# Kernel optimization log

Hardware: AMD Instinct MI355X
Metric: run time of the kernel (lower is better)

Reference implementation:

```python
import jax, jax.numpy as jnp
import numpy as np

CANVAS = 28      # canvas_size
P = 2            # num_paths
S = 3            # num_segments
PPP = S * 3 + 1  # points_per_path = 10
T = 32           # samples per bezier segment
SS = 2           # 2x2 = 4 supersamples per pixel (num_samples=4)
MARGIN = 2.0
TAU = 0.5        # anti-alias softness of coverage (differentiable rasterizer)
LATENT = 64
HIDDEN = 512


def _leaky(x):
    return jnp.where(x >= 0, x, 0.2 * x)


def _encoder(x, e_w1, e_b1, e_w2, e_b2, w_mu, b_mu, w_lv, b_lv):
    h = x.reshape(x.shape[0], -1)
    h = _leaky(h @ e_w1 + e_b1)
    h = _leaky(h @ e_w2 + e_b2)
    return h @ w_mu + b_mu, h @ w_lv + b_lv


def _decoder(z, d_w1, d_b1, d_w2, d_b2, p_w, p_b, wd_w, wd_b, a_w, a_b):
    B = z.shape[0]
    h = jax.nn.selu(z @ d_w1 + d_b1)
    h = jax.nn.selu(h @ d_w2 + d_b2)
    pts = jnp.tanh(h @ p_w + p_b).reshape(B, P, PPP, 2)
    pts = pts * (CANVAS / 2 - MARGIN) + CANVAS / 2
    # stack overlapping cubic segments: [B,P,S,4,2]
    cp = jnp.stack([pts[:, :, 3 * s:3 * s + 4, :] for s in range(S)], axis=2)
    widths = jax.nn.sigmoid(h @ wd_w + wd_b) * 2.0 + 1.0  # [B,P]
    alphas = jax.nn.sigmoid(h @ a_w + a_b)                # [B,P]
    return cp, widths, alphas


def _render(cp, widths, alphas):
    """Differentiable supersampled stroke rasterizer, white bg, 1-x flip."""
    B = cp.shape[0]
    t = (jnp.arange(T, dtype=cp.dtype) + 0.5) / T
    basis = jnp.stack([(1 - t) ** 3, 3 * t * (1 - t) ** 2,
                       3 * t ** 2 * (1 - t), t ** 3], axis=-1)  # [T,4]
    curve = jnp.einsum('tk,bpskc->bpstc', basis, cp).reshape(B, P, S * T, 2)
    # supersampled pixel sample positions (pixel units)
    coords = (jnp.arange(CANVAS * SS, dtype=cp.dtype) + 0.5) / SS
    ys, xs = jnp.meshgrid(coords, coords, indexing='ij')
    samp = jnp.stack([xs, ys], -1).reshape(-1, 2)  # [N,2], N = (28*2)^2
    # [B,P,N,M] squared distances -> min over curve samples
    d2 = jnp.sum((samp[None, None, :, None, :] - curve[:, :, None, :, :]) ** 2, -1)
    d = jnp.sqrt(jnp.min(d2, axis=-1) + 1e-12)  # [B,P,N]
    cov = jax.nn.sigmoid((widths[..., None] * 0.5 - d) / TAU)
    a = alphas[..., None] * cov                 # per-path ink opacity
    val = jnp.prod(1.0 - a, axis=1)             # composite black ink over bg=1.0
    img = val.reshape(B, CANVAS, SS, CANVAS, SS).mean(axis=(2, 4))
    return 1.0 - img[:, None]                   # [B,1,H,W]


def setup_inputs() -> dict:
    key = jax.random.key(0)
    ks = jax.random.split(key, 24)
    n = lambda k, s, sc=0.05: (jax.random.normal(k, s, dtype=jnp.float32) * sc)
    B = 128
    return {
        'x': jax.random.uniform(ks[0], (B, 1, 28, 28), dtype=jnp.float32),
        'eps': jax.random.normal(ks[1], (B, LATENT), dtype=jnp.float32),
        'e_w1': n(ks[2], (784, 256)), 'e_b1': jnp.zeros(256),
        'e_w2': n(ks[3], (256, 256)), 'e_b2': jnp.zeros(256),
        'w_mu': n(ks[4], (256, LATENT)), 'b_mu': jnp.zeros(LATENT),
        'w_lv': n(ks[5], (256, LATENT)), 'b_lv': jnp.zeros(LATENT),
        'd_w1': n(ks[6], (LATENT, HIDDEN)), 'd_b1': jnp.zeros(HIDDEN),
        'd_w2': n(ks[7], (HIDDEN, HIDDEN)), 'd_b2': jnp.zeros(HIDDEN),
        'p_w': n(ks[8], (HIDDEN, P * PPP * 2)), 'p_b': jnp.zeros(P * PPP * 2),
        'wd_w': n(ks[9], (HIDDEN, P)), 'wd_b': jnp.zeros(P),
        'a_w': n(ks[10], (HIDDEN, P)), 'a_b': jnp.zeros(P),
    }


def reference(x, eps, e_w1, e_b1, e_w2, e_b2, w_mu, b_mu, w_lv, b_lv,
              d_w1, d_b1, d_w2, d_b2, p_w, p_b, wd_w, wd_b, a_w, a_b):
    mu, logvar = _encoder(x, e_w1, e_b1, e_w2, e_b2, w_mu, b_mu, w_lv, b_lv)
    z = mu + eps * jnp.exp(0.5 * logvar)
    cp, widths, alphas = _decoder(z, d_w1, d_b1, d_w2, d_b2,
                                  p_w, p_b, wd_w, wd_b, a_w, a_b)
    rendered = _render(cp, widths, alphas)
    return rendered, mu, logvar, cp, widths, alphas
```

## Files before the change

kernel.cpp:

```cpp
#include <hip/hip_runtime.h>
#include <hip/hip_bf16.h>
#include <hip/hip_fp16.h>
#include <math.h>

#define REND_OFF 0
#define MU_OFF   100352
#define LV_OFF   108544
#define CP_OFF   116736
#define W_OFF    122880
#define A_OFF    123136

#define Q_W1 0
#define Q_W2 25600
#define Q_ML 33792
#define Q_D1 37888
#define Q_D2 41984
#define Q_H  74752
#define Q_TOT 78848

typedef _Float16 half2_t __attribute__((ext_vector_type(2)));

__device__ __forceinline__ float leakyf(float x) {
    return x >= 0.f ? x : 0.2f * x;
}
__device__ __forceinline__ float seluf(float x) {
    const float sc = 1.0507009873554805f;
    const float al = 1.6732632423543772f;
    return x > 0.f ? sc * x : sc * al * expm1f(x);
}
__device__ __forceinline__ float sigmoidf(float x) {
    return 1.f / (1.f + expf(-x));
}
__device__ __forceinline__ unsigned pkh(float a, float b) {
    __half ha = __float2half(a), hb = __float2half(b);
    return (unsigned)__half_as_ushort(ha) | ((unsigned)__half_as_ushort(hb) << 16);
}
__device__ __forceinline__ half2_t as_h2(unsigned u) {
    union { unsigned u; half2_t h; } c; c.u = u; return c.h;
}
__device__ __forceinline__ float dot2(unsigned a, unsigned w, float acc) {
#if __has_builtin(__builtin_amdgcn_fdot2)
    return __builtin_amdgcn_fdot2(as_h2(a), as_h2(w), acc, false);
#else
    half2_t ah = as_h2(a), wh = as_h2(w);
    acc = fmaf((float)ah[0], (float)wh[0], acc);
    return fmaf((float)ah[1], (float)wh[1], acc);
#endif
}

__global__ __launch_bounds__(256) void conv_w(
    const float* __restrict__ e_w1, const float* __restrict__ e_w2,
    const float* __restrict__ w_mu, const float* __restrict__ w_lv,
    const float* __restrict__ d_w1, const float* __restrict__ d_w2,
    const float* __restrict__ p_w,  const float* __restrict__ wd_w,
    const float* __restrict__ a_w,  uint4* __restrict__ wsq)
{
    int t = blockIdx.x * 256 + threadIdx.x;
    if (t >= Q_TOT) return;
    float lo[4], hi[4];
    if (t < Q_W2) {
        int q = t, k2 = q >> 6, j4 = q & 63;
        int k0 = 2 * k2, c0 = 4 * j4;
        #pragma unroll
        for (int c = 0; c < 4; ++c) {
            lo[c] = (k0     < 784) ? e_w1[k0 * 256 + c0 + c] : 0.f;
            hi[c] = (k0 + 1 < 784) ? e_w1[(k0 + 1) * 256 + c0 + c] : 0.f;
        }
    } else if (t < Q_ML) {
        int q = t - Q_W2, k2 = q >> 6, j4 = q & 63;
        int k0 = 2 * k2, c0 = 4 * j4;
        #pragma unroll
        for (int c = 0; c < 4; ++c) {
            lo[c] = e_w2[k0 * 256 + c0 + c];
            hi[c] = e_w2[(k0 + 1) * 256 + c0 + c];
        }
    } else if (t < Q_D1) {
        int q = t - Q_ML, k2 = q >> 5, j4 = q & 31;
        int k0 = 2 * k2, c0 = 4 * j4;
        #pragma unroll
        for (int c = 0; c < 4; ++c) {
            int cc = c0 + c;
            lo[c] = (cc < 64) ? w_mu[k0 * 64 + cc] : w_lv[k0 * 64 + cc - 64];
            hi[c] = (cc < 64) ? w_mu[(k0 + 1) * 64 + cc]
                              : w_lv[(k0 + 1) * 64 + cc - 64];
        }
    } else if (t < Q_D2) {
        int q = t - Q_D1, k2 = q >> 7, j4 = q & 127;
        int k0 = 2 * k2, c0 = 4 * j4;
        #pragma unroll
        for (int c = 0; c < 4; ++c) {
            lo[c] = d_w1[k0 * 512 + c0 + c];
            hi[c] = d_w1[(k0 + 1) * 512 + c0 + c];
        }
    } else if (t < Q_H) {
        int q = t - Q_D2, k2 = q >> 7, j4 = q & 127;
        int k0 = 2 * k2, c0 = 4 * j4;
        #pragma unroll
        for (int c = 0; c < 4; ++c) {
            lo[c] = d_w2[k0 * 512 + c0 + c];
            hi[c] = d_w2[(k0 + 1) * 512 + c0 + c];
        }
    } else {
        int q = t - Q_H, k2 = q >> 4, j4 = q & 15;
        int k0 = 2 * k2, c0 = 4 * j4;
        #pragma unroll
        for (int c = 0; c < 4; ++c) {
            int cc = c0 + c;
            lo[c] = (cc < 40) ? p_w[k0 * 40 + cc]
                  : (cc < 42) ? wd_w[k0 * 2 + cc - 40]
                  : (cc < 44) ? a_w[k0 * 2 + cc - 42] : 0.f;
            hi[c] = (cc < 40) ? p_w[(k0 + 1) * 40 + cc]
                  : (cc < 42) ? wd_w[(k0 + 1) * 2 + cc - 40]
                  : (cc < 44) ? a_w[(k0 + 1) * 2 + cc - 42] : 0.f;
        }
    }
    uint4 u;
    u.x = pkh(lo[0], hi[0]);
    u.y = pkh(lo[1], hi[1]);
    u.z = pkh(lo[2], hi[2]);
    u.w = pkh(lo[3], hi[3]);
    wsq[t] = u;
}

template<int N, int JG, int S, int Ks>
__device__ __forceinline__ void hgemm(const uint4* __restrict__ wq,
                                      const unsigned* __restrict__ xu,
                                      float* __restrict__ red, int tid)
{
    constexpr int NTp = N + 4;
    const int jg = tid % JG, ks = tid / JG;
    const uint4* wp = wq + (ks * Ks) * (N / 4) + jg;
    const unsigned* xp = xu + ks * Ks;
    float a0 = 0.f, a1 = 0.f, a2 = 0.f, a3 = 0.f;
    #pragma unroll 8
    for (int kk = 0; kk < Ks; ++kk) {
        uint4 w = wp[kk * (N / 4)];
        unsigned av = xp[kk];
        a0 = dot2(av, w.x, a0);
        a1 = dot2(av, w.y, a1);
        a2 = dot2(av, w.z, a2);
        a3 = dot2(av, w.w, a3);
    }
    *(float4*)&red[ks * NTp + 4 * jg] = make_float4(a0, a1, a2, a3);
}

template<int N, int S, int ACT>
__device__ __forceinline__ void reduce_pack(const float* __restrict__ red,
                                            const float* __restrict__ bias,
                                            unsigned* __restrict__ Cu, int tid)
{
    constexpr int NTp = N + 4;
    if (tid < N / 2) {
        int j0 = 2 * tid;
        float s0 = bias[j0], s1 = bias[j0 + 1];
        #pragma unroll
        for (int si = 0; si < S; ++si) {
            s0 += red[si * NTp + j0];
            s1 += red[si * NTp + j0 + 1];
        }
        if (ACT == 1) { s0 = leakyf(s0); s1 = leakyf(s1); }
        else          { s0 = seluf(s0);  s1 = seluf(s1);  }
        Cu[tid] = pkh(s0, s1);
    }
}

__global__ __launch_bounds__(1024) void vae_mlp(
    const float* __restrict__ x,    const float* __restrict__ eps,
    const float* __restrict__ e_b1, const float* __restrict__ e_b2,
    const float* __restrict__ b_mu, const float* __restrict__ b_lv,
    const float* __restrict__ d_b1, const float* __restrict__ d_b2,
    const float* __restrict__ p_b,  const float* __restrict__ wd_b,
    const float* __restrict__ a_b,
    const uint4* __restrict__ wsq,  float* __restrict__ out)
{
    const int b   = blockIdx.x;
    const int tid = threadIdx.x;

    __shared__ __align__(16) unsigned xs[400];
    __shared__ __align__(16) unsigned h1u[128];
    __shared__ __align__(16) unsigned h2u[128];
    __shared__ __align__(16) unsigned zu[32];
    __shared__ __align__(16) unsigned d1u[256];
    __shared__ __align__(16) unsigned d2u[256];
    __shared__ float mulv[128];
    __shared__ float pts[40];
    __shared__ __align__(16) float red[4352];

    if (tid < 400) {
        int k0 = 2 * tid;
        float x0 = (k0     < 784) ? x[b * 784 + k0] : 0.f;
        float x1 = (k0 + 1 < 784) ? x[b * 784 + k0 + 1] : 0.f;
        xs[tid] = pkh(x0, x1);
    }
    __syncthreads();

    hgemm<256, 64, 16, 25>(wsq + Q_W1, xs, red, tid);
    __syncthreads();
    reduce_pack<256, 16, 1>(red, e_b1, h1u, tid);
    __syncthreads();

    hgemm<256, 64, 16, 8>(wsq + Q_W2, h1u, red, tid);
    __syncthreads();
    reduce_pack<256, 16, 1>(red, e_b2, h2u, tid);
    __syncthreads();

    hgemm<128, 32, 32, 4>(wsq + Q_ML, h2u, red, tid);
    __syncthreads();
    if (tid < 64) {
        int u0 = 2 * tid;
        float s0 = (u0 < 64) ? b_mu[u0] : b_lv[u0 - 64];
        float s1 = (u0 < 64) ? b_mu[u0 + 1] : b_lv[u0 + 1 - 64];
        #pragma unroll
        for (int si = 0; si < 32; ++si) {
            s0 += red[si * 132 + u0];
            s1 += red[si * 132 + u0 + 1];
        }
        mulv[u0] = s0; mulv[u0 + 1] = s1;
        int base = (u0 < 64) ? MU_OFF : LV_OFF;
        out[base + b * 64 + (u0 & 63)]     = s0;
        out[base + b * 64 + (u0 & 63) + 1] = s1;
    }
    __syncthreads();
    if (tid < 32) {
        int j0 = 2 * tid;
        float z0 = fmaf(eps[b * 64 + j0],     expf(0.5f * mulv[64 + j0]),     mulv[j0]);
        float z1 = fmaf(eps[b * 64 + j0 + 1], expf(0.5f * mulv[64 + j0 + 1]), mulv[j0 + 1]);
        zu[tid] = pkh(z0, z1);
    }
    __syncthreads();

    hgemm<512, 128, 8, 4>(wsq + Q_D1, zu, red, tid);
    __syncthreads();
    reduce_pack<512, 8, 2>(red, d_b1, d1u, tid);
    __syncthreads();

    hgemm<512, 128, 8, 32>(wsq + Q_D2, d1u, red, tid);
    __syncthreads();
    reduce_pack<512, 8, 2>(red, d_b2, d2u, tid);
    __syncthreads();

    hgemm<64, 16, 64, 4>(wsq + Q_H, d2u, red, tid);
    __syncthreads();
    if (tid < 44) {
        float s = 0.f;
        #pragma unroll
        for (int si = 0; si < 64; ++si) s += red[si * 68 + tid];
        if (tid < 40) {
            pts[tid] = tanhf(s + p_b[tid]) * 12.f + 14.f;
        } else if (tid < 42) {
            out[W_OFF + b * 2 + (tid - 40)] =
                sigmoidf(s + wd_b[tid - 40]) * 2.f + 1.f;
        } else {
            out[A_OFF + b * 2 + (tid - 42)] = sigmoidf(s + a_b[tid - 42]);
        }
    }
    __syncthreads();

    if (tid < 48) {
        int p = tid / 24, rem = tid % 24;
        int s = rem / 8, kc = rem % 8;
        int k = kc >> 1, c = kc & 1;
        out[CP_OFF + b * 48 + tid] = pts[p * 20 + (3 * s + k) * 2 + c];
    }
}

__global__ __launch_bounds__(256) void vae_render(float* __restrict__ out)
{
    const int b   = blockIdx.x;
    const int q   = blockIdx.y;
    const int tid = threadIdx.x;

    __shared__ float2 cur[192];
    __shared__ float  wa[4];

    if (tid < 192) {
        int p = tid / 96;
        int m = tid % 96;
        int s = m / 32;
        int t = m % 32;
        float u  = (t + 0.5f) * (1.f / 32.f);
        float v  = 1.f - u;
        float b0 = v * v * v;
        float b1 = 3.f * u * v * v;
        float b2 = 3.f * u * u * v;
        float b3 = u * u * u;
        const float* cp = out + CP_OFF + b * 48 + p * 24 + s * 8;
        float cx = b0 * cp[0] + b1 * cp[2] + b2 * cp[4] + b3 * cp[6];
        float cy = b0 * cp[1] + b1 * cp[3] + b2 * cp[5] + b3 * cp[7];
        cur[tid] = make_float2(cx, cy);
    } else if (tid < 196) {
        int i = tid - 192;
        wa[i] = (i < 2) ? 0.5f * out[W_OFF + b * 2 + i]
                        : out[A_OFF + b * 2 + (i - 2)];
    }
    __syncthreads();

    if (tid < 196) {
        int Y = tid / 28, X = tid - Y * 28;
        float px0 = X + 0.25f;
        float py0 = (7 * q + Y) + 0.25f;

        float mA[4] = {1e30f, 1e30f, 1e30f, 1e30f};
        float mB[4] = {1e30f, 1e30f, 1e30f, 1e30f};
        #pragma unroll 4
        for (int m = 0; m < 96; ++m) {
            float2 c = cur[m];
            float dx0 = px0 - c.x, dy0 = py0 - c.y;
            float dx1 = dx0 + 0.5f, dy1 = dy0 + 0.5f;
            float xx0 = dx0 * dx0, xx1 = dx1 * dx1;
            float yy0 = dy0 * dy0, yy1 = dy1 * dy1;
            mA[0] = fminf(mA[0], xx0 + yy0);
            mA[1] = fminf(mA[1], xx1 + yy0);
            mA[2] = fminf(mA[2], xx0 + yy1);
            mA[3] = fminf(mA[3], xx1 + yy1);
        }
        #pragma unroll 4
        for (int m = 96; m < 192; ++m) {
            float2 c = cur[m];
            float dx0 = px0 - c.x, dy0 = py0 - c.y;
            float dx1 = dx0 + 0.5f, dy1 = dy0 + 0.5f;
            float xx0 = dx0 * dx0, xx1 = dx1 * dx1;
            float yy0 = dy0 * dy0, yy1 = dy1 * dy1;
            mB[0] = fminf(mB[0], xx0 + yy0);
            mB[1] = fminf(mB[1], xx1 + yy0);
            mB[2] = fminf(mB[2], xx0 + yy1);
            mB[3] = fminf(mB[3], xx1 + yy1);
        }

        const float w0 = wa[0], w1 = wa[1], a0 = wa[2], a1 = wa[3];
        float v = 0.f;
        #pragma unroll
        for (int s = 0; s < 4; ++s) {
            float d0 = sqrtf(mA[s] + 1e-12f);
            float d1 = sqrtf(mB[s] + 1e-12f);
            float c0 = a0 / (1.f + expf(-2.f * (w0 - d0)));
            float c1 = a1 / (1.f + expf(-2.f * (w1 - d1)));
            v += (1.f - c0) * (1.f - c1);
        }
        out[REND_OFF + b * 784 + (7 * q + Y) * 28 + X] = 1.f - 0.25f * v;
    }
}

extern "C" void kernel_launch(void* const* d_in, const int* in_sizes, int n_in,
                              void* d_out, int out_size, void* d_ws, size_t ws_size,
                              hipStream_t stream) {
    const float* x    = (const float*)d_in[0];
    const float* eps  = (const float*)d_in[1];
    const float* e_w1 = (const float*)d_in[2];
    const float* e_b1 = (const float*)d_in[3];
    const float* e_w2 = (const float*)d_in[4];
    const float* e_b2 = (const float*)d_in[5];
    const float* w_mu = (const float*)d_in[6];
    const float* b_mu = (const float*)d_in[7];
    const float* w_lv = (const float*)d_in[8];
    const float* b_lv = (const float*)d_in[9];
    const float* d_w1 = (const float*)d_in[10];
    const float* d_b1 = (const float*)d_in[11];
    const float* d_w2 = (const float*)d_in[12];
    const float* d_b2 = (const float*)d_in[13];
    const float* p_w  = (const float*)d_in[14];
    const float* p_b  = (const float*)d_in[15];
    const float* wd_w = (const float*)d_in[16];
    const float* wd_b = (const float*)d_in[17];
    const float* a_w  = (const float*)d_in[18];
    const float* a_b  = (const float*)d_in[19];
    float* out = (float*)d_out;
    uint4* wsq = (uint4*)d_ws;

    hipLaunchKernelGGL(conv_w, dim3((Q_TOT + 255) / 256), dim3(256), 0, stream,
                       e_w1, e_w2, w_mu, w_lv, d_w1, d_w2, p_w, wd_w, a_w, wsq);
    hipLaunchKernelGGL(vae_mlp, dim3(128), dim3(1024), 0, stream,
                       x, eps, e_b1, e_b2, b_mu, b_lv, d_b1, d_b2,
                       p_b, wd_b, a_b, wsq, out);
    hipLaunchKernelGGL(vae_render, dim3(128, 4), dim3(256), 0, stream, out);
}
```

Measured before the change: 123.7 us.

## Quantize MLP weights to per-column int8 instead of fp16 packed pairs

Replaces the fp16 weight conversion with a per-column symmetric int8 quantization kernel that stores a scale per output column, then runs the MLP GEMMs with unsigned-offset int8 weights against fp32 activations and corrects the offset using the activation sum. The aim is to halve the weight bytes each of the 128 blocks streams from cache/memory. In exchange, the inner loop does more ALU work: byte extraction, int-to-float converts and four scalar FMAs in place of each fdot2. The conversion kernel also gains a per-column max reduction, and int8 weights bring extra quantization error.

```diff
diff --git a/kernel.cpp b/kernel.cpp
--- a/kernel.cpp
+++ b/kernel.cpp
@@ -1,6 +1,4 @@
 #include <hip/hip_runtime.h>
-#include <hip/hip_bf16.h>
-#include <hip/hip_fp16.h>
 #include <math.h>
 
 #define REND_OFF 0
@@ -10,15 +8,20 @@
 #define W_OFF    122880
 #define A_OFF    123136
 
-#define Q_W1 0
-#define Q_W2 25600
-#define Q_ML 33792
-#define Q_D1 37888
-#define Q_D2 41984
-#define Q_H  74752
-#define Q_TOT 78848
-
-typedef _Float16 half2_t __attribute__((ext_vector_type(2)));
+#define U_W1 0
+#define U_W2 53248
+#define U_ML 69632
+#define U_D1 77824
+#define U_D2 86016
+#define U_H  151552
+#define SCOFF 159744
+#define B_W1 0
+#define B_W2 256
+#define B_ML 512
+#define B_D1 640
+#define B_D2 1152
+#define B_H  1664
+#define NCOLS 1728
 
 __device__ __forceinline__ float leakyf(float x) {
     return x >= 0.f ? x : 0.2f * x;
@@ -31,136 +34,109 @@
 __device__ __forceinline__ float sigmoidf(float x) {
     return 1.f / (1.f + expf(-x));
 }
-__device__ __forceinline__ unsigned pkh(float a, float b) {
-    __half ha = __float2half(a), hb = __float2half(b);
-    return (unsigned)__half_as_ushort(ha) | ((unsigned)__half_as_ushort(hb) << 16);
-}
-__device__ __forceinline__ half2_t as_h2(unsigned u) {
-    union { unsigned u; half2_t h; } c; c.u = u; return c.h;
-}
-__device__ __forceinline__ float dot2(unsigned a, unsigned w, float acc) {
-#if __has_builtin(__builtin_amdgcn_fdot2)
-    return __builtin_amdgcn_fdot2(as_h2(a), as_h2(w), acc, false);
-#else
-    half2_t ah = as_h2(a), wh = as_h2(w);
-    acc = fmaf((float)ah[0], (float)wh[0], acc);
-    return fmaf((float)ah[1], (float)wh[1], acc);
-#endif
-}
-
-__global__ __launch_bounds__(256) void conv_w(
+__device__ __forceinline__ float ub0(unsigned w) { return (float)(w & 0xffu); }
+__device__ __forceinline__ float ub1(unsigned w) { return (float)((w >> 8) & 0xffu); }
+__device__ __forceinline__ float ub2(unsigned w) { return (float)((w >> 16) & 0xffu); }
+__device__ __forceinline__ float ub3(unsigned w) { return (float)(w >> 24); }
+
+__global__ __launch_bounds__(256) void conv_q(
     const float* __restrict__ e_w1, const float* __restrict__ e_w2,
     const float* __restrict__ w_mu, const float* __restrict__ w_lv,
     const float* __restrict__ d_w1, const float* __restrict__ d_w2,
     const float* __restrict__ p_w,  const float* __restrict__ wd_w,
-    const float* __restrict__ a_w,  uint4* __restrict__ wsq)
-{
-    int t = blockIdx.x * 256 + threadIdx.x;
-    if (t >= Q_TOT) return;
-    float lo[4], hi[4];
-    if (t < Q_W2) {
-        int q = t, k2 = q >> 6, j4 = q & 63;
-        int k0 = 2 * k2, c0 = 4 * j4;
-        #pragma unroll
-        for (int c = 0; c < 4; ++c) {
-            lo[c] = (k0     < 784) ? e_w1[k0 * 256 + c0 + c] : 0.f;
-            hi[c] = (k0 + 1 < 784) ? e_w1[(k0 + 1) * 256 + c0 + c] : 0.f;
-        }
-    } else if (t < Q_ML) {
-        int q = t - Q_W2, k2 = q >> 6, j4 = q & 63;
-        int k0 = 2 * k2, c0 = 4 * j4;
-        #pragma unroll
-        for (int c = 0; c < 4; ++c) {
-            lo[c] = e_w2[k0 * 256 + c0 + c];
-            hi[c] = e_w2[(k0 + 1) * 256 + c0 + c];
-        }
-    } else if (t < Q_D1) {
-        int q = t - Q_ML, k2 = q >> 5, j4 = q & 31;
-        int k0 = 2 * k2, c0 = 4 * j4;
-        #pragma unroll
-        for (int c = 0; c < 4; ++c) {
-            int cc = c0 + c;
-            lo[c] = (cc < 64) ? w_mu[k0 * 64 + cc] : w_lv[k0 * 64 + cc - 64];
-            hi[c] = (cc < 64) ? w_mu[(k0 + 1) * 64 + cc]
-                              : w_lv[(k0 + 1) * 64 + cc - 64];
-        }
-    } else if (t < Q_D2) {
-        int q = t - Q_D1, k2 = q >> 7, j4 = q & 127;
-        int k0 = 2 * k2, c0 = 4 * j4;
-        #pragma unroll
-        for (int c = 0; c < 4; ++c) {
-            lo[c] = d_w1[k0 * 512 + c0 + c];
-            hi[c] = d_w1[(k0 + 1) * 512 + c0 + c];
-        }
-    } else if (t < Q_H) {
-        int q = t - Q_D2, k2 = q >> 7, j4 = q & 127;
-        int k0 = 2 * k2, c0 = 4 * j4;
-        #pragma unroll
-        for (int c = 0; c < 4; ++c) {
-            lo[c] = d_w2[k0 * 512 + c0 + c];
-            hi[c] = d_w2[(k0 + 1) * 512 + c0 + c];
-        }
-    } else {
-        int q = t - Q_H, k2 = q >> 4, j4 = q & 15;
-        int k0 = 2 * k2, c0 = 4 * j4;
-        #pragma unroll
-        for (int c = 0; c < 4; ++c) {
-            int cc = c0 + c;
-            lo[c] = (cc < 40) ? p_w[k0 * 40 + cc]
-                  : (cc < 42) ? wd_w[k0 * 2 + cc - 40]
-                  : (cc < 44) ? a_w[k0 * 2 + cc - 42] : 0.f;
-            hi[c] = (cc < 40) ? p_w[(k0 + 1) * 40 + cc]
-                  : (cc < 42) ? wd_w[(k0 + 1) * 2 + cc - 40]
-                  : (cc < 44) ? a_w[(k0 + 1) * 2 + cc - 42] : 0.f;
-        }
-    }
-    uint4 u;
-    u.x = pkh(lo[0], hi[0]);
-    u.y = pkh(lo[1], hi[1]);
-    u.z = pkh(lo[2], hi[2]);
-    u.w = pkh(lo[3], hi[3]);
-    wsq[t] = u;
-}
-
-template<int N, int JG, int S, int Ks>
-__device__ __forceinline__ void hgemm(const uint4* __restrict__ wq,
-                                      const unsigned* __restrict__ xu,
-                                      float* __restrict__ red, int tid)
+    const float* __restrict__ a_w,  unsigned* __restrict__ wsu)
+{
+    const int col  = blockIdx.x * 4 + (threadIdx.x >> 6);
+    const int lane = threadIdx.x & 63;
+    if (col >= NCOLS) return;
+
+    int K, G, N, base, c;
+    const float* src = nullptr;
+    int stride = 0;
+    if (col < 256)       { c = col;        K = 784; G = 208; N = 256; base = U_W1; src = e_w1 + c; stride = 256; }
+    else if (col < 512)  { c = col - 256;  K = 256; G = 64;  N = 256; base = U_W2; src = e_w2 + c; stride = 256; }
+    else if (col < 640)  { c = col - 512;  K = 256; G = 64;  N = 128; base = U_ML;
+                           src = (c < 64) ? (w_mu + c) : (w_lv + c - 64); stride = 64; }
+    else if (col < 1152) { c = col - 640;  K = 64;  G = 16;  N = 512; base = U_D1; src = d_w1 + c; stride = 512; }
+    else if (col < 1664) { c = col - 1152; K = 512; G = 128; N = 512; base = U_D2; src = d_w2 + c; stride = 512; }
+    else                 { c = col - 1664; K = 512; G = 128; N = 64;  base = U_H;
+                           if (c < 40)      { src = p_w + c;        stride = 40; }
+                           else if (c < 42) { src = wd_w + (c - 40); stride = 2; }
+                           else if (c < 44) { src = a_w + (c - 42);  stride = 2; }
+                           else             { src = nullptr; } }
+
+    float m = 0.f;
+    if (src) {
+        for (int k = lane; k < K; k += 64)
+            m = fmaxf(m, fabsf(src[k * stride]));
+    }
+    #pragma unroll
+    for (int d = 1; d < 64; d <<= 1)
+        m = fmaxf(m, __shfl_xor(m, d));
+    const float inv = (m > 0.f) ? 127.f / m : 0.f;
+    const float scale = m / 127.f;
+
+    const int colN = col - ((col < 256) ? 0 : (col < 512) ? 256 : (col < 640) ? 512
+                     : (col < 1152) ? 640 : (col < 1664) ? 1152 : 1664);
+    for (int g = lane; g < G; g += 64) {
+        unsigned u = 0;
+        #pragma unroll
+        for (int e = 0; e < 4; ++e) {
+            int k = 4 * g + e;
+            float w = (src && k < K) ? src[k * stride] : 0.f;
+            float qf = rintf(w * inv);
+            qf = fminf(127.f, fmaxf(-127.f, qf));
+            unsigned b = (unsigned)((int)qf + 128);
+            u |= b << (8 * e);
+        }
+        wsu[base + g * N + colN] = u;
+    }
+    if (lane == 0)
+        ((float*)(wsu + SCOFF))[col] = scale;
+}
+
+template<int N, int JG, int S, int G>
+__device__ __forceinline__ void i8gemm(const uint4* __restrict__ wq,
+                                       const float* __restrict__ xf,
+                                       float* __restrict__ red, int tid)
 {
     constexpr int NTp = N + 4;
     const int jg = tid % JG, ks = tid / JG;
-    const uint4* wp = wq + (ks * Ks) * (N / 4) + jg;
-    const unsigned* xp = xu + ks * Ks;
-    float a0 = 0.f, a1 = 0.f, a2 = 0.f, a3 = 0.f;
+    const uint4* wp = wq + (ks * G) * (N / 4) + jg;
+    const float4* xp = (const float4*)xf + ks * G;
+    float a0 = 0.f, a1 = 0.f, a2 = 0.f, a3 = 0.f, sx = 0.f;
     #pragma unroll 8
-    for (int kk = 0; kk < Ks; ++kk) {
-        uint4 w = wp[kk * (N / 4)];
-        unsigned av = xp[kk];
-        a0 = dot2(av, w.x, a0);
-        a1 = dot2(av, w.y, a1);
-        a2 = dot2(av, w.z, a2);
-        a3 = dot2(av, w.w, a3);
-    }
-    *(float4*)&red[ks * NTp + 4 * jg] = make_float4(a0, a1, a2, a3);
+    for (int g = 0; g < G; ++g) {
+        uint4 w = wp[g * (N / 4)];
+        float4 xv = xp[g];
+        sx += (xv.x + xv.y) + (xv.z + xv.w);
+        a0 = fmaf(ub0(w.x), xv.x, a0); a0 = fmaf(ub1(w.x), xv.y, a0);
+        a0 = fmaf(ub2(w.x), xv.z, a0); a0 = fmaf(ub3(w.x), xv.w, a0);
+        a1 = fmaf(ub0(w.y), xv.x, a1); a1 = fmaf(ub1(w.y), xv.y, a1);
+        a1 = fmaf(ub2(w.y), xv.z, a1); a1 = fmaf(ub3(w.y), xv.w, a1);
+        a2 = fmaf(ub0(w.z), xv.x, a2); a2 = fmaf(ub1(w.z), xv.y, a2);
+        a2 = fmaf(ub2(w.z), xv.z, a2); a2 = fmaf(ub3(w.z), xv.w, a2);
+        a3 = fmaf(ub0(w.w), xv.x, a3); a3 = fmaf(ub1(w.w), xv.y, a3);
+        a3 = fmaf(ub2(w.w), xv.z, a3); a3 = fmaf(ub3(w.w), xv.w, a3);
+    }
+    const float bias = -128.f * sx;
+    *(float4*)&red[ks * NTp + 4 * jg] =
+        make_float4(a0 + bias, a1 + bias, a2 + bias, a3 + bias);
 }
 
 template<int N, int S, int ACT>
-__device__ __forceinline__ void reduce_pack(const float* __restrict__ red,
-                                            const float* __restrict__ bias,
-                                            unsigned* __restrict__ Cu, int tid)
+__device__ __forceinline__ void reduce_i8(const float* __restrict__ red,
+                                          const float* __restrict__ scl,
+                                          const float* __restrict__ bias,
+                                          float* __restrict__ Cf, int tid)
 {
     constexpr int NTp = N + 4;
-    if (tid < N / 2) {
-        int j0 = 2 * tid;
-        float s0 = bias[j0], s1 = bias[j0 + 1];
-        #pragma unroll
-        for (int si = 0; si < S; ++si) {
-            s0 += red[si * NTp + j0];
-            s1 += red[si * NTp + j0 + 1];
-        }
-        if (ACT == 1) { s0 = leakyf(s0); s1 = leakyf(s1); }
-        else          { s0 = seluf(s0);  s1 = seluf(s1);  }
-        Cu[tid] = pkh(s0, s1);
+    if (tid < N) {
+        float s = 0.f;
+        #pragma unroll
+        for (int si = 0; si < S; ++si) s += red[si * NTp + tid];
+        float v = fmaf(scl[tid], s, bias[tid]);
+        Cf[tid] = (ACT == 1) ? leakyf(v) : seluf(v);
     }
 }
 
@@ -171,80 +147,71 @@
     const float* __restrict__ d_b1, const float* __restrict__ d_b2,
     const float* __restrict__ p_b,  const float* __restrict__ wd_b,
     const float* __restrict__ a_b,
-    const uint4* __restrict__ wsq,  float* __restrict__ out)
+    const unsigned* __restrict__ wsu, float* __restrict__ out)
 {
     const int b   = blockIdx.x;
     const int tid = threadIdx.x;
 
-    __shared__ __align__(16) unsigned xs[400];
-    __shared__ __align__(16) unsigned h1u[128];
-    __shared__ __align__(16) unsigned h2u[128];
-    __shared__ __align__(16) unsigned zu[32];
-    __shared__ __align__(16) unsigned d1u[256];
-    __shared__ __align__(16) unsigned d2u[256];
+    __shared__ __align__(16) float xs[832];
+    __shared__ __align__(16) float h1f[256];
+    __shared__ __align__(16) float h2f[256];
+    __shared__ __align__(16) float zf[64];
+    __shared__ __align__(16) float d1f[512];
+    __shared__ __align__(16) float d2f[512];
     __shared__ float mulv[128];
     __shared__ float pts[40];
+    __shared__ float scl[NCOLS];
     __shared__ __align__(16) float red[4352];
 
-    if (tid < 400) {
-        int k0 = 2 * tid;
-        float x0 = (k0     < 784) ? x[b * 784 + k0] : 0.f;
-        float x1 = (k0 + 1 < 784) ? x[b * 784 + k0 + 1] : 0.f;
-        xs[tid] = pkh(x0, x1);
-    }
-    __syncthreads();
-
-    hgemm<256, 64, 16, 25>(wsq + Q_W1, xs, red, tid);
-    __syncthreads();
-    reduce_pack<256, 16, 1>(red, e_b1, h1u, tid);
-    __syncthreads();
-
-    hgemm<256, 64, 16, 8>(wsq + Q_W2, h1u, red, tid);
-    __syncthreads();
-    reduce_pack<256, 16, 1>(red, e_b2, h2u, tid);
-    __syncthreads();
-
-    hgemm<128, 32, 32, 4>(wsq + Q_ML, h2u, red, tid);
+    if (tid < 832) xs[tid] = (tid < 784) ? x[b * 784 + tid] : 0.f;
+    for (int i = tid; i < NCOLS; i += 1024)
+        scl[i] = ((const float*)(wsu + SCOFF))[i];
+    __syncthreads();
+
+    i8gemm<256, 64, 16, 13>((const uint4*)(wsu + U_W1), xs, red, tid);
+    __syncthreads();
+    reduce_i8<256, 16, 1>(red, scl + B_W1, e_b1, h1f, tid);
+    __syncthreads();
+
+    i8gemm<256, 64, 16, 4>((const uint4*)(wsu + U_W2), h1f, red, tid);
+    __syncthreads();
+    reduce_i8<256, 16, 1>(red, scl + B_W2, e_b2, h2f, tid);
+    __syncthreads();
+
+    i8gemm<128, 32, 32, 2>((const uint4*)(wsu + U_ML), h2f, red, tid);
+    __syncthreads();
+    if (tid < 128) {
+        float s = 0.f;
+        #pragma unroll
+        for (int si = 0; si < 32; ++si) s += red[si * 132 + tid];
+        float v = fmaf(scl[B_ML + tid], s,
+                       (tid < 64) ? b_mu[tid] : b_lv[tid - 64]);
+        mulv[tid] = v;
+        out[(tid < 64 ? MU_OFF : LV_OFF) + b * 64 + (tid & 63)] = v;
+    }
     __syncthreads();
     if (tid < 64) {
-        int u0 = 2 * tid;
-        float s0 = (u0 < 64) ? b_mu[u0] : b_lv[u0 - 64];
-        float s1 = (u0 < 64) ? b_mu[u0 + 1] : b_lv[u0 + 1 - 64];
-        #pragma unroll
-        for (int si = 0; si < 32; ++si) {
-            s0 += red[si * 132 + u0];
-            s1 += red[si * 132 + u0 + 1];
-        }
-        mulv[u0] = s0; mulv[u0 + 1] = s1;
-        int base = (u0 < 64) ? MU_OFF : LV_OFF;
-        out[base + b * 64 + (u0 & 63)]     = s0;
-        out[base + b * 64 + (u0 & 63) + 1] = s1;
-    }
-    __syncthreads();
-    if (tid < 32) {
-        int j0 = 2 * tid;
-        float z0 = fmaf(eps[b * 64 + j0],     expf(0.5f * mulv[64 + j0]),     mulv[j0]);
-        float z1 = fmaf(eps[b * 64 + j0 + 1], expf(0.5f * mulv[64 + j0 + 1]), mulv[j0 + 1]);
-        zu[tid] = pkh(z0, z1);
-    }
-    __syncthreads();
-
-    hgemm<512, 128, 8, 4>(wsq + Q_D1, zu, red, tid);
-    __syncthreads();
-    reduce_pack<512, 8, 2>(red, d_b1, d1u, tid);
-    __syncthreads();
-
-    hgemm<512, 128, 8, 32>(wsq + Q_D2, d1u, red, tid);
-    __syncthreads();
-    reduce_pack<512, 8, 2>(red, d_b2, d2u, tid);
-    __syncthreads();
-
-    hgemm<64, 16, 64, 4>(wsq + Q_H, d2u, red, tid);
+        zf[tid] = fmaf(eps[b * 64 + tid], expf(0.5f * mulv[64 + tid]), mulv[tid]);
+    }
+    __syncthreads();
+
+    i8gemm<512, 128, 8, 2>((const uint4*)(wsu + U_D1), zf, red, tid);
+    __syncthreads();
+    reduce_i8<512, 8, 2>(red, scl + B_D1, d_b1, d1f, tid);
+    __syncthreads();
+
+    i8gemm<512, 128, 8, 16>((const uint4*)(wsu + U_D2), d1f, red, tid);
+    __syncthreads();
+    reduce_i8<512, 8, 2>(red, scl + B_D2, d_b2, d2f, tid);
+    __syncthreads();
+
+    i8gemm<64, 16, 64, 2>((const uint4*)(wsu + U_H), d2f, red, tid);
     __syncthreads();
     if (tid < 44) {
         float s = 0.f;
         #pragma unroll
         for (int si = 0; si < 64; ++si) s += red[si * 68 + tid];
+        s *= scl[B_H + tid];
         if (tid < 40) {
             pts[tid] = tanhf(s + p_b[tid]) * 12.f + 14.f;
         } else if (tid < 42) {
@@ -365,12 +332,12 @@
     const float* a_w  = (const float*)d_in[18];
     const float* a_b  = (const float*)d_in[19];
     float* out = (float*)d_out;
-    uint4* wsq = (uint4*)d_ws;
-
-    hipLaunchKernelGGL(conv_w, dim3((Q_TOT + 255) / 256), dim3(256), 0, stream,
-                       e_w1, e_w2, w_mu, w_lv, d_w1, d_w2, p_w, wd_w, a_w, wsq);
+    unsigned* wsu = (unsigned*)d_ws;
+
+    hipLaunchKernelGGL(conv_q, dim3(432), dim3(256), 0, stream,
+                       e_w1, e_w2, w_mu, w_lv, d_w1, d_w2, p_w, wd_w, a_w, wsu);
     hipLaunchKernelGGL(vae_mlp, dim3(128), dim3(1024), 0, stream,
                        x, eps, e_b1, e_b2, b_mu, b_lv, d_b1, d_b2,
-                       p_b, wd_b, a_b, wsq, out);
+                       p_b, wd_b, a_b, wsu, out);
     hipLaunchKernelGGL(vae_render, dim3(128, 4), dim3(256), 0, stream, out);
 }
```

New measurement: 133.9 us. 8.2% more time.

## Replace shared-memory split-K reduction with wave shuffle reductions in MLP kernel

Applied to the files above, without the earlier changes.

Each hgemm now gives a wavefront a group of output columns and splits K across the lanes of that wave, then reduces the partial sums with __shfl_xor butterflies instead of writing them to shared memory and running a separate reduce pass. This removes one __syncthreads and one LDS round trip per layer, and the bias vectors are preloaded into shared memory once at the start. In exchange, the shuffle steps add cross-lane traffic, and the per-lane weight access pattern changes, which may hurt coalescing.

```diff
diff --git a/kernel.cpp b/kernel.cpp
--- a/kernel.cpp
+++ b/kernel.cpp
@@ -17,6 +17,17 @@
 #define Q_D2 41984
 #define Q_H  74752
 #define Q_TOT 78848
+
+#define SB_E1 0
+#define SB_E2 256
+#define SB_MU 512
+#define SB_LV 576
+#define SB_D1 640
+#define SB_D2 1152
+#define SB_P  1664
+#define SB_WD 1704
+#define SB_A  1706
+#define SB_TOT 1708
 
 typedef _Float16 half2_t __attribute__((ext_vector_type(2)));
 
@@ -122,15 +133,17 @@
     wsq[t] = u;
 }
 
-template<int N, int JG, int S, int Ks>
-__device__ __forceinline__ void hgemm(const uint4* __restrict__ wq,
-                                      const unsigned* __restrict__ xu,
-                                      float* __restrict__ red, int tid)
+template<int N, int JW, int Ks>
+__device__ __forceinline__ void hgemm_w(const uint4* __restrict__ wq,
+                                        const unsigned* __restrict__ xu,
+                                        float (&a)[4], int tid)
 {
-    constexpr int NTp = N + 4;
-    const int jg = tid % JG, ks = tid / JG;
-    const uint4* wp = wq + (ks * Ks) * (N / 4) + jg;
-    const unsigned* xp = xu + ks * Ks;
+    const int l  = tid & 63;
+    const int wv = tid >> 6;
+    const int jg = wv * JW + (l % JW);
+    const int g  = l / JW;
+    const uint4* wp = wq + (g * Ks) * (N / 4) + jg;
+    const unsigned* xp = xu + g * Ks;
     float a0 = 0.f, a1 = 0.f, a2 = 0.f, a3 = 0.f;
     #pragma unroll 8
     for (int kk = 0; kk < Ks; ++kk) {
@@ -141,27 +154,14 @@
         a2 = dot2(av, w.z, a2);
         a3 = dot2(av, w.w, a3);
     }
-    *(float4*)&red[ks * NTp + 4 * jg] = make_float4(a0, a1, a2, a3);
-}
-
-template<int N, int S, int ACT>
-__device__ __forceinline__ void reduce_pack(const float* __restrict__ red,
-                                            const float* __restrict__ bias,
-                                            unsigned* __restrict__ Cu, int tid)
-{
-    constexpr int NTp = N + 4;
-    if (tid < N / 2) {
-        int j0 = 2 * tid;
-        float s0 = bias[j0], s1 = bias[j0 + 1];
-        #pragma unroll
-        for (int si = 0; si < S; ++si) {
-            s0 += red[si * NTp + j0];
-            s1 += red[si * NTp + j0 + 1];
-        }
-        if (ACT == 1) { s0 = leakyf(s0); s1 = leakyf(s1); }
-        else          { s0 = seluf(s0);  s1 = seluf(s1);  }
-        Cu[tid] = pkh(s0, s1);
-    }
+    #pragma unroll
+    for (int m = JW; m < 64; m <<= 1) {
+        a0 += __shfl_xor(a0, m);
+        a1 += __shfl_xor(a1, m);
+        a2 += __shfl_xor(a2, m);
+        a3 += __shfl_xor(a3, m);
+    }
+    a[0] = a0; a[1] = a1; a[2] = a2; a[3] = a3;
 }
 
 __global__ __launch_bounds__(1024) void vae_mlp(
@@ -175,6 +175,8 @@
 {
     const int b   = blockIdx.x;
     const int tid = threadIdx.x;
+    const int l   = tid & 63;
+    const int wv  = tid >> 6;
 
     __shared__ __align__(16) unsigned xs[400];
     __shared__ __align__(16) unsigned h1u[128];
@@ -184,7 +186,7 @@
     __shared__ __align__(16) unsigned d2u[256];
     __shared__ float mulv[128];
     __shared__ float pts[40];
-    __shared__ __align__(16) float red[4352];
+    __shared__ float sb[SB_TOT];
 
     if (tid < 400) {
         int k0 = 2 * tid;
@@ -192,33 +194,53 @@
         float x1 = (k0 + 1 < 784) ? x[b * 784 + k0 + 1] : 0.f;
         xs[tid] = pkh(x0, x1);
     }
-    __syncthreads();
-
-    hgemm<256, 64, 16, 25>(wsq + Q_W1, xs, red, tid);
-    __syncthreads();
-    reduce_pack<256, 16, 1>(red, e_b1, h1u, tid);
-    __syncthreads();
-
-    hgemm<256, 64, 16, 8>(wsq + Q_W2, h1u, red, tid);
-    __syncthreads();
-    reduce_pack<256, 16, 1>(red, e_b2, h2u, tid);
-    __syncthreads();
-
-    hgemm<128, 32, 32, 4>(wsq + Q_ML, h2u, red, tid);
-    __syncthreads();
-    if (tid < 64) {
-        int u0 = 2 * tid;
-        float s0 = (u0 < 64) ? b_mu[u0] : b_lv[u0 - 64];
-        float s1 = (u0 < 64) ? b_mu[u0 + 1] : b_lv[u0 + 1 - 64];
-        #pragma unroll
-        for (int si = 0; si < 32; ++si) {
-            s0 += red[si * 132 + u0];
-            s1 += red[si * 132 + u0 + 1];
-        }
-        mulv[u0] = s0; mulv[u0 + 1] = s1;
-        int base = (u0 < 64) ? MU_OFF : LV_OFF;
-        out[base + b * 64 + (u0 & 63)]     = s0;
-        out[base + b * 64 + (u0 & 63) + 1] = s1;
+    for (int i = tid; i < SB_TOT; i += 1024) {
+        float v;
+        if (i < 256)       v = e_b1[i];
+        else if (i < 512)  v = e_b2[i - 256];
+        else if (i < 576)  v = b_mu[i - 512];
+        else if (i < 640)  v = b_lv[i - 576];
+        else if (i < 1152) v = d_b1[i - 640];
+        else if (i < 1664) v = d_b2[i - 1152];
+        else if (i < 1704) v = p_b[i - 1664];
+        else if (i < 1706) v = wd_b[i - 1704];
+        else               v = a_b[i - 1706];
+        sb[i] = v;
+    }
+    __syncthreads();
+
+    float a[4];
+
+    hgemm_w<256, 4, 25>(wsq + Q_W1, xs, a, tid);
+    if (l < 4) {
+        int jg = wv * 4 + l, c0 = 4 * jg;
+        h1u[2 * jg]     = pkh(leakyf(a[0] + sb[SB_E1 + c0]),
+                              leakyf(a[1] + sb[SB_E1 + c0 + 1]));
+        h1u[2 * jg + 1] = pkh(leakyf(a[2] + sb[SB_E1 + c0 + 2]),
+                              leakyf(a[3] + sb[SB_E1 + c0 + 3]));
+    }
+    __syncthreads();
+
+    hgemm_w<256, 4, 8>(wsq + Q_W2, h1u, a, tid);
+    if (l < 4) {
+        int jg = wv * 4 + l, c0 = 4 * jg;
+        h2u[2 * jg]     = pkh(leakyf(a[0] + sb[SB_E2 + c0]),
+                              leakyf(a[1] + sb[SB_E2 + c0 + 1]));
+        h2u[2 * jg + 1] = pkh(leakyf(a[2] + sb[SB_E2 + c0 + 2]),
+                              leakyf(a[3] + sb[SB_E2 + c0 + 3]));
+    }
+    __syncthreads();
+
+    hgemm_w<128, 2, 4>(wsq + Q_ML, h2u, a, tid);
+    if (l < 2) {
+        int jg = wv * 2 + l, c0 = 4 * jg;
+        #pragma unroll
+        for (int e = 0; e < 4; ++e) {
+            int cc = c0 + e;
+            float v = a[e] + ((cc < 64) ? sb[SB_MU + cc] : sb[SB_LV + cc - 64]);
+            mulv[cc] = v;
+            out[((cc < 64) ? MU_OFF : LV_OFF) + b * 64 + (cc & 63)] = v;
+        }
     }
     __syncthreads();
     if (tid < 32) {
@@ -229,29 +251,41 @@
     }
     __syncthreads();
 
-    hgemm<512, 128, 8, 4>(wsq + Q_D1, zu, red, tid);
-    __syncthreads();
-    reduce_pack<512, 8, 2>(red, d_b1, d1u, tid);
-    __syncthreads();
-
-    hgemm<512, 128, 8, 32>(wsq + Q_D2, d1u, red, tid);
-    __syncthreads();
-    reduce_pack<512, 8, 2>(red, d_b2, d2u, tid);
-    __syncthreads();
-
-    hgemm<64, 16, 64, 4>(wsq + Q_H, d2u, red, tid);
-    __syncthreads();
-    if (tid < 44) {
-        float s = 0.f;
-        #pragma unroll
-        for (int si = 0; si < 64; ++si) s += red[si * 68 + tid];
-        if (tid < 40) {
-            pts[tid] = tanhf(s + p_b[tid]) * 12.f + 14.f;
-        } else if (tid < 42) {
-            out[W_OFF + b * 2 + (tid - 40)] =
-                sigmoidf(s + wd_b[tid - 40]) * 2.f + 1.f;
-        } else {
-            out[A_OFF + b * 2 + (tid - 42)] = sigmoidf(s + a_b[tid - 42]);
+    hgemm_w<512, 8, 4>(wsq + Q_D1, zu, a, tid);
+    if (l < 8) {
+        int jg = wv * 8 + l, c0 = 4 * jg;
+        d1u[2 * jg]     = pkh(seluf(a[0] + sb[SB_D1 + c0]),
+                              seluf(a[1] + sb[SB_D1 + c0 + 1]));
+        d1u[2 * jg + 1] = pkh(seluf(a[2] + sb[SB_D1 + c0 + 2]),
+                              seluf(a[3] + sb[SB_D1 + c0 + 3]));
+    }
+    __syncthreads();
+
+    hgemm_w<512, 8, 32>(wsq + Q_D2, d1u, a, tid);
+    if (l < 8) {
+        int jg = wv * 8 + l, c0 = 4 * jg;
+        d2u[2 * jg]     = pkh(seluf(a[0] + sb[SB_D2 + c0]),
+                              seluf(a[1] + sb[SB_D2 + c0 + 1]));
+        d2u[2 * jg + 1] = pkh(seluf(a[2] + sb[SB_D2 + c0 + 2]),
+                              seluf(a[3] + sb[SB_D2 + c0 + 3]));
+    }
+    __syncthreads();
+
+    hgemm_w<64, 1, 4>(wsq + Q_H, d2u, a, tid);
+    if (l == 0) {
+        int c0 = 4 * wv;
+        #pragma unroll
+        for (int e = 0; e < 4; ++e) {
+            int cc = c0 + e;
+            if (cc < 40) {
+                pts[cc] = tanhf(a[e] + sb[SB_P + cc]) * 12.f + 14.f;
+            } else if (cc < 42) {
+                out[W_OFF + b * 2 + (cc - 40)] =
+                    sigmoidf(a[e] + sb[SB_WD + cc - 40]) * 2.f + 1.f;
+            } else if (cc < 44) {
+                out[A_OFF + b * 2 + (cc - 42)] =
+                    sigmoidf(a[e] + sb[SB_A + cc - 42]);
+            }
         }
     }
     __syncthreads();
```

After: 127.2 us. +2.8%, slower.

## Fuse stroke rendering into the MLP kernel to drop the render launch

Applied to the files above, without the earlier changes.

Moves the Bezier curve evaluation and supersampled rendering into the tail of the per-sample MLP kernel. Curve points and width/alpha values now come straight from shared memory instead of being re-read from global output. Each 1024-thread block renders all 784 pixels itself. This removes one kernel launch and the global round-trip, at the cost of fewer blocks doing the render work (128 instead of 512) and a bigger shared-memory footprint for the MLP kernel.

```diff
diff --git a/kernel.cpp b/kernel.cpp
--- a/kernel.cpp
+++ b/kernel.cpp
@@ -184,7 +184,9 @@
     __shared__ __align__(16) unsigned d2u[256];
     __shared__ float mulv[128];
     __shared__ float pts[40];
+    __shared__ float wa[4];
     __shared__ __align__(16) float red[4352];
+    __shared__ float2 cur[192];
 
     if (tid < 400) {
         int k0 = 2 * tid;
@@ -248,10 +250,13 @@
         if (tid < 40) {
             pts[tid] = tanhf(s + p_b[tid]) * 12.f + 14.f;
         } else if (tid < 42) {
-            out[W_OFF + b * 2 + (tid - 40)] =
-                sigmoidf(s + wd_b[tid - 40]) * 2.f + 1.f;
+            float wd = sigmoidf(s + wd_b[tid - 40]) * 2.f + 1.f;
+            out[W_OFF + b * 2 + (tid - 40)] = wd;
+            wa[tid - 40] = 0.5f * wd;
         } else {
-            out[A_OFF + b * 2 + (tid - 42)] = sigmoidf(s + a_b[tid - 42]);
+            float al = sigmoidf(s + a_b[tid - 42]);
+            out[A_OFF + b * 2 + (tid - 42)] = al;
+            wa[tid - 42 + 2] = al;
         }
     }
     __syncthreads();
@@ -262,43 +267,27 @@
         int k = kc >> 1, c = kc & 1;
         out[CP_OFF + b * 48 + tid] = pts[p * 20 + (3 * s + k) * 2 + c];
     }
-}
-
-__global__ __launch_bounds__(256) void vae_render(float* __restrict__ out)
-{
-    const int b   = blockIdx.x;
-    const int q   = blockIdx.y;
-    const int tid = threadIdx.x;
-
-    __shared__ float2 cur[192];
-    __shared__ float  wa[4];
-
-    if (tid < 192) {
-        int p = tid / 96;
-        int m = tid % 96;
-        int s = m / 32;
-        int t = m % 32;
+    if (tid >= 64 && tid < 256) {
+        int i = tid - 64;
+        int p = i / 96, m = i % 96;
+        int s = m / 32, t = m % 32;
         float u  = (t + 0.5f) * (1.f / 32.f);
         float v  = 1.f - u;
         float b0 = v * v * v;
         float b1 = 3.f * u * v * v;
         float b2 = 3.f * u * u * v;
         float b3 = u * u * u;
-        const float* cp = out + CP_OFF + b * 48 + p * 24 + s * 8;
-        float cx = b0 * cp[0] + b1 * cp[2] + b2 * cp[4] + b3 * cp[6];
-        float cy = b0 * cp[1] + b1 * cp[3] + b2 * cp[5] + b3 * cp[7];
-        cur[tid] = make_float2(cx, cy);
-    } else if (tid < 196) {
-        int i = tid - 192;
-        wa[i] = (i < 2) ? 0.5f * out[W_OFF + b * 2 + i]
-                        : out[A_OFF + b * 2 + (i - 2)];
-    }
-    __syncthreads();
-
-    if (tid < 196) {
+        const float* q = pts + p * 20 + 3 * s * 2;
+        float cx = b0 * q[0] + b1 * q[2] + b2 * q[4] + b3 * q[6];
+        float cy = b0 * q[1] + b1 * q[3] + b2 * q[5] + b3 * q[7];
+        cur[i] = make_float2(cx, cy);
+    }
+    __syncthreads();
+
+    if (tid < 784) {
         int Y = tid / 28, X = tid - Y * 28;
         float px0 = X + 0.25f;
-        float py0 = (7 * q + Y) + 0.25f;
+        float py0 = Y + 0.25f;
 
         float mA[4] = {1e30f, 1e30f, 1e30f, 1e30f};
         float mB[4] = {1e30f, 1e30f, 1e30f, 1e30f};
@@ -327,17 +316,17 @@
             mB[3] = fminf(mB[3], xx1 + yy1);
         }
 
-        const float w0 = wa[0], w1 = wa[1], a0 = wa[2], a1 = wa[3];
+        const float w0 = wa[0], w1 = wa[1], al0 = wa[2], al1 = wa[3];
         float v = 0.f;
         #pragma unroll
         for (int s = 0; s < 4; ++s) {
             float d0 = sqrtf(mA[s] + 1e-12f);
             float d1 = sqrtf(mB[s] + 1e-12f);
-            float c0 = a0 / (1.f + expf(-2.f * (w0 - d0)));
-            float c1 = a1 / (1.f + expf(-2.f * (w1 - d1)));
+            float c0 = al0 / (1.f + expf(-2.f * (w0 - d0)));
+            float c1 = al1 / (1.f + expf(-2.f * (w1 - d1)));
             v += (1.f - c0) * (1.f - c1);
         }
-        out[REND_OFF + b * 784 + (7 * q + Y) * 28 + X] = 1.f - 0.25f * v;
+        out[REND_OFF + b * 784 + Y * 28 + X] = 1.f - 0.25f * v;
     }
 }
 
@@ -372,5 +361,4 @@
     hipLaunchKernelGGL(vae_mlp, dim3(128), dim3(1024), 0, stream,
                        x, eps, e_b1, e_b2, b_mu, b_lv, d_b1, d_b2,
                        p_b, wd_b, a_b, wsq, out);
-    hipLaunchKernelGGL(vae_render, dim3(128, 4), dim3(256), 0, stream, out);
-}
+}
```

New measurement: 129.7 us. +4.8%, slower.
